# Kernel optimization log

Hardware: AMD Instinct MI355X
Metric: run time of the kernel (lower is better)

## Reference

```python
import jax, jax.numpy as jnp
import numpy as np

B, H, W = 64, 480, 640      # batch, cartesian iris image size
PH, PW = 64, 512            # polar grid
FS, NF = 15, 7              # BSIF filter size / count


def setup_inputs() -> dict:
    key = jax.random.key(0)
    k1, k2, k3, k4, k5, k6 = jax.random.split(key, 6)
    image = jax.random.uniform(k1, (B, 1, H, W), jnp.float32)
    pcx = jax.random.uniform(k2, (B,), jnp.float32, 280.0, 360.0)
    pcy = jax.random.uniform(k3, (B,), jnp.float32, 200.0, 280.0)
    pr = jax.random.uniform(k4, (B,), jnp.float32, 30.0, 60.0)
    ir = jax.random.uniform(k5, (B,), jnp.float32, 90.0, 130.0)
    pupil_xyr = jnp.stack([pcx, pcy, pr], axis=-1)
    iris_xyr = jnp.stack([pcx, pcy, ir], axis=-1)
    filter_mat = jax.random.normal(k6, (FS, FS, NF), jnp.float32)
    return {"image": image, "pupil_xyr": pupil_xyr, "iris_xyr": iris_xyr,
            "filter_mat": filter_mat}


def _bilinear_sample(img, gx, gy):
    """torch.nn.functional.grid_sample, mode=bilinear, align_corners=False,
    padding_mode=zeros. img [B,C,H,W]; gx,gy [B,Hg,Wg] normalized coords."""
    _, _, Hi, Wi = img.shape
    x = ((gx + 1.0) * Wi - 1.0) / 2.0
    y = ((gy + 1.0) * Hi - 1.0) / 2.0
    x0 = jnp.floor(x); y0 = jnp.floor(y)
    wx = x - x0; wy = y - y0

    def gather(ix, iy):
        valid = (ix >= 0) & (ix < Wi) & (iy >= 0) & (iy < Hi)
        ixc = jnp.clip(ix, 0, Wi - 1).astype(jnp.int32)
        iyc = jnp.clip(iy, 0, Hi - 1).astype(jnp.int32)
        v = jax.vmap(lambda im, yy, xx: im[:, yy, xx])(img, iyc, ixc)  # [B,C,Hg,Wg]
        return v * valid[:, None].astype(img.dtype)

    v00 = gather(x0, y0); v01 = gather(x0 + 1, y0)
    v10 = gather(x0, y0 + 1); v11 = gather(x0 + 1, y0 + 1)
    wx = wx[:, None]; wy = wy[:, None]  # [B,1,Hg,Wg]
    return (v00 * (1 - wx) * (1 - wy) + v01 * wx * (1 - wy)
            + v10 * (1 - wx) * wy + v11 * wx * wy)


def _forward(image, pupil_xyr, iris_xyr, filter_mat):
    image_scaled = image * 255.0
    _, _, Hc, Wc = image_scaled.shape

    # --- cartToPol: polar sampling grid from pupil/iris circles ---
    theta = 2.0 * jnp.pi * jnp.arange(1, PW + 1, dtype=jnp.float32) / PW
    cosT, sinT = jnp.cos(theta), jnp.sin(theta)                     # [PW]
    pxc = pupil_xyr[:, 0:1] + pupil_xyr[:, 2:3] * cosT[None]        # [B,PW]
    pyc = pupil_xyr[:, 1:2] + pupil_xyr[:, 2:3] * sinT[None]
    ixc = iris_xyr[:, 0:1] + iris_xyr[:, 2:3] * cosT[None]
    iyc = iris_xyr[:, 1:2] + iris_xyr[:, 2:3] * sinT[None]
    radius = jnp.linspace(0.0, 1.0, PH)[:, None]                    # [PH,1]
    xg = (1 - radius)[None] * pxc[:, None, :] + radius[None] * ixc[:, None, :]  # [B,PH,PW]
    yg = (1 - radius)[None] * pyc[:, None, :] + radius[None] * iyc[:, None, :]
    x = jnp.clip(xg, 0.0, Wc - 1.0)
    y = jnp.clip(yg, 0.0, Hc - 1.0)
    x_norm = x / (Wc - 1) * 2.0 - 1.0
    y_norm = y / (Hc - 1) * 2.0 - 1.0
    # module's custom grid_sample pre-transform (half-pixel re-normalization)
    gx = ((x_norm + 1.0) / 2.0 * Wc - 0.5) / (Wc - 1) * 2.0 - 1.0
    gy = ((y_norm + 1.0) / 2.0 * Hc - 0.5) / (Hc - 1) * 2.0 - 1.0
    image_polar = _bilinear_sample(image_scaled, gx, gy)            # [B,1,PH,PW]

    # --- getCodes: toroidal wrap pad + conv filter bank ---
    r = FS // 2
    img_wrap = jnp.pad(image_polar, ((0, 0), (0, 0), (r, r), (r, r)), mode="wrap")
    # torch: moveaxis(filter[None], 3, 0) -> (NF,1,FS,FS), then flip along dim 0
    weight = jnp.flip(jnp.transpose(filter_mat, (2, 0, 1))[:, None, :, :], axis=0)
    codes = jax.lax.conv_general_dilated(
        img_wrap, weight, window_strides=(1, 1), padding="VALID",
        dimension_numbers=("NCHW", "OIHW", "NCHW"))                 # [B,NF,PH,PW]

    # --- gram matrix ---
    a, b, c, d = codes.shape
    feats = codes.reshape(a * b, c * d)
    gram = (feats @ feats.T) / (a * b * c * d)                      # [a*b, a*b]
    return codes, gram, image_polar


def reference(image, pupil_xyr, iris_xyr, filter_mat):
    return _forward(image, pupil_xyr, iris_xyr, filter_mat)
```

## Files before the change

### kernel.cpp

```cpp
#include <hip/hip_runtime.h>
#include <math.h>

#define BB 64
#define HH 480
#define WW 640
#define PH 64
#define PW 512
#define FS 15
#define NF 7
#define RR 7
#define GD 448
#define KTOT 32768

#define GSPL 16
#define KPB (KTOT / GSPL)
#define GSTK 64
#define GNST (KPB / GSTK)
#define GPLW 72

#define FSPL 32
#define FKPB (KTOT / FSPL)
#define GBK 32
#define GNB (FKPB / GBK)
#define PLW 40

#define CJT 32
#define CSP 52
#define CSPD 26
#define CSROWS 79
#define CSY 46

static constexpr long CODES_N = (long)BB * NF * PH * PW;
static constexpr long GRAM_N  = (long)GD * GD;
static constexpr long POLAR_N = (long)BB * PH * PW;
static constexpr size_t BF_BYTES   = (size_t)GD * KTOT * 2;
static constexpr size_t PART_BYTES = (size_t)GSPL * GRAM_N * 4;

typedef __bf16    bf16x4   __attribute__((ext_vector_type(4)));
typedef __bf16    bf16x8   __attribute__((ext_vector_type(8)));
typedef _Float16  f16x8    __attribute__((ext_vector_type(8)));
typedef float     floatx4  __attribute__((ext_vector_type(4)));
typedef float     floatx16 __attribute__((ext_vector_type(16)));

__constant__ int c_by[28] = {0,0,0,0,0,0,0, 1,1,1,1,1,1, 2,2,2,2,2, 3,3,3,3, 4,4,4, 5,5, 6};
__constant__ int c_bx[28] = {0,1,2,3,4,5,6, 1,2,3,4,5,6, 2,3,4,5,6, 3,4,5,6, 4,5,6, 5,6, 6};

__global__ __launch_bounds__(256) void polar_kernel(
        const float* __restrict__ img,
        const float* __restrict__ pupil,
        const float* __restrict__ iris,
        float* __restrict__ polar) {
    int t = blockIdx.x * 256 + threadIdx.x;
    if (t >= (int)POLAR_N) return;
    int j = t & (PW - 1);
    int i = (t >> 9) & (PH - 1);
    int b = t >> 15;

    float theta = 6.2831855f * (float)(j + 1) / (float)PW;
    float s, c;
    __sincosf(theta, &s, &c);

    float pcx = pupil[b * 3 + 0], pcy = pupil[b * 3 + 1], pr = pupil[b * 3 + 2];
    float icx = iris[b * 3 + 0],  icy = iris[b * 3 + 1],  ir = iris[b * 3 + 2];

    float px = pcx + pr * c;
    float py = pcy + pr * s;
    float ix = icx + ir * c;
    float iy = icy + ir * s;

    float r = (float)i / 63.0f;
    float xg = (1.0f - r) * px + r * ix;
    float yg = (1.0f - r) * py + r * iy;

    float x = fminf(fmaxf(xg, 0.0f), (float)(WW - 1));
    float y = fminf(fmaxf(yg, 0.0f), (float)(HH - 1));

    float xn = x / (float)(WW - 1) * 2.0f - 1.0f;
    float gx = ((xn + 1.0f) / 2.0f * (float)WW - 0.5f) / (float)(WW - 1) * 2.0f - 1.0f;
    float xs = ((gx + 1.0f) * (float)WW - 1.0f) / 2.0f;

    float yn = y / (float)(HH - 1) * 2.0f - 1.0f;
    float gy = ((yn + 1.0f) / 2.0f * (float)HH - 0.5f) / (float)(HH - 1) * 2.0f - 1.0f;
    float ys = ((gy + 1.0f) * (float)HH - 1.0f) / 2.0f;

    float x0f = floorf(xs), y0f = floorf(ys);
    float wx = xs - x0f, wy = ys - y0f;
    int x0 = (int)x0f, y0 = (int)y0f;

    const float* im = img + (size_t)b * (HH * WW);
    float v00 = 0.f, v01 = 0.f, v10 = 0.f, v11 = 0.f;
    bool xv0 = (x0 >= 0) & (x0 < WW);
    bool xv1 = (x0 + 1 >= 0) & (x0 + 1 < WW);
    bool yv0 = (y0 >= 0) & (y0 < HH);
    bool yv1 = (y0 + 1 >= 0) & (y0 + 1 < HH);
    if (xv0 & yv0) v00 = im[(size_t)y0 * WW + x0];
    if (xv1 & yv0) v01 = im[(size_t)y0 * WW + x0 + 1];
    if (xv0 & yv1) v10 = im[(size_t)(y0 + 1) * WW + x0];
    if (xv1 & yv1) v11 = im[(size_t)(y0 + 1) * WW + x0 + 1];

    float val = v00 * (1.0f - wx) * (1.0f - wy) + v01 * wx * (1.0f - wy)
              + v10 * (1.0f - wx) * wy          + v11 * wx * wy;
    polar[t] = val * 255.0f;
}

__global__ __launch_bounds__(256) void conv_mfma_kernel(
        const float* __restrict__ polar,
        const float* __restrict__ fm,
        float* __restrict__ codes,
        __bf16* __restrict__ cbf) {
    __shared__ __align__(16) _Float16 stg[CSROWS * CSP];
    __shared__ __align__(16) float outBuf[NF * 16 * CJT];

    int b  = blockIdx.x >> 4;
    int j0 = (blockIdx.x & 15) * CJT;
    int tid  = threadIdx.x;
    int lane = tid & 63;
    int w    = tid >> 6;

    const float* pb = polar + (size_t)b * (PH * PW);

    for (int e = tid; e < CSROWS * CSY; e += 256) {
        int r = e / CSY;
        int y = e - r * CSY;
        int grow = (r - RR) & (PH - 1);
        int gcol = (j0 - RR + y) & (PW - 1);
        stg[r * CSP + y] = (_Float16)pb[grow * PW + gcol];
    }

    uint4* Wb = (uint4*)outBuf;
    for (int slot = tid; slot < 512; slot += 256) {
        int s  = slot >> 6;
        int l  = slot & 63;
        int du = l >> 5;
        int v0 = ((l >> 4) & 1) * 8;
        int n  = l & 15;
        int jd = (n >= NF) ? 1 : 0;
        int o  = n - NF * jd;
        int u  = 2 * s + du;
        f16x8 vv = {};
        #pragma unroll
        for (int e2 = 0; e2 < 8; ++e2) {
            int v  = v0 + e2;
            int vp = v - jd;
            float wv = 0.0f;
            if (n < 2 * NF && u < FS && vp >= 0 && vp < FS)
                wv = fm[(u * FS + vp) * NF + (NF - 1 - o)];
            vv[e2] = (_Float16)wv;
        }
        Wb[slot] = *(const uint4*)&vv;
    }
    __syncthreads();

    f16x8 Wreg[8];
    #pragma unroll
    for (int s = 0; s < 8; ++s)
        Wreg[s] = *(const f16x8*)&Wb[s * 64 + lane];
    __syncthreads();

    const unsigned int* stg32 = (const unsigned int*)stg;
    int mrow = lane & 15;
    int du   = lane >> 5;
    int v0h  = ((lane >> 4) & 1) * 4;
    int n    = lane & 15;
    int jd   = (n >= NF) ? 1 : 0;
    int o    = n - NF * jd;
    int g4   = lane >> 4;

    for (int it = 0; it < 4; ++it) {
        int i0 = it * 16;
        int rbase = i0 + mrow + du;
        floatx4 acc0 = {}, acc1 = {}, acc2 = {}, acc3 = {};
        #pragma unroll
        for (int s = 0; s < 8; ++s) {
            int dbase = CSPD * (rbase + 2 * s) + 4 * w + v0h;
            uint2 u01 = *(const uint2*)&stg32[dbase + 0];
            uint2 u23 = *(const uint2*)&stg32[dbase + 2];
            uint2 u45 = *(const uint2*)&stg32[dbase + 4];
            uint2 u67 = *(const uint2*)&stg32[dbase + 6];
            unsigned int ud0 = u01.x, ud1 = u01.y, ud2 = u23.x, ud3 = u23.y;
            unsigned int ud4 = u45.x, ud5 = u45.y, ud6 = u67.x, ud7 = u67.y;
            uint4 a0 = make_uint4(ud0, ud1, ud2, ud3);
            uint4 a1 = make_uint4(ud1, ud2, ud3, ud4);
            uint4 a2 = make_uint4(ud2, ud3, ud4, ud5);
            uint4 a3 = make_uint4(ud3, ud4, ud5, ud6);
            (void)ud7;
            acc0 = __builtin_amdgcn_mfma_f32_16x16x32_f16(*(const f16x8*)&a0, Wreg[s], acc0, 0, 0, 0);
            acc1 = __builtin_amdgcn_mfma_f32_16x16x32_f16(*(const f16x8*)&a1, Wreg[s], acc1, 0, 0, 0);
            acc2 = __builtin_amdgcn_mfma_f32_16x16x32_f16(*(const f16x8*)&a2, Wreg[s], acc2, 0, 0, 0);
            acc3 = __builtin_amdgcn_mfma_f32_16x16x32_f16(*(const f16x8*)&a3, Wreg[s], acc3, 0, 0, 0);
        }
        if (n < 2 * NF) {
            #pragma unroll
            for (int r = 0; r < 4; ++r) {
                int orow = (o * 16 + (4 * g4 + r)) * CJT;
                outBuf[orow + 2 * (w * 4 + 0) + jd] = acc0[r];
                outBuf[orow + 2 * (w * 4 + 1) + jd] = acc1[r];
                outBuf[orow + 2 * (w * 4 + 2) + jd] = acc2[r];
                outBuf[orow + 2 * (w * 4 + 3) + jd] = acc3[r];
            }
        }
        __syncthreads();
        for (int g = tid; g < NF * 16 * (CJT / 4); g += 256) {
            int oo  = g >> 7;
            int rem = g & 127;
            int il  = rem >> 3;
            int j4  = rem & 7;
            float4 v = *(const float4*)&outBuf[(oo * 16 + il) * CJT + j4 * 4];
            size_t gbase = (((size_t)b * NF + oo) * PH + i0 + il) * PW + j0 + j4 * 4;
            *(float4*)&codes[gbase] = v;
            if (cbf) {
                bf16x4 bv;
                bv[0] = (__bf16)v.x; bv[1] = (__bf16)v.y;
                bv[2] = (__bf16)v.z; bv[3] = (__bf16)v.w;
                *(bf16x4*)&cbf[gbase] = bv;
            }
        }
        __syncthreads();
    }
}

__global__ __launch_bounds__(256) void gram_bf_kernel(
        const __bf16* __restrict__ feats,
        float* __restrict__ partials) {
    __shared__ __bf16 Ab[2][64][GPLW];
    __shared__ __bf16 Bb[2][64][GPLW];

    int pi = blockIdx.x;
    int by = c_by[pi], bx = c_bx[pi];
    int p0 = by * 64, q0 = bx * 64;
    size_t kbase = (size_t)blockIdx.y * KPB;

    int tid = threadIdx.x;
    int lane = tid & 63;
    int w = tid >> 6;
    int wr = w >> 1, wc = w & 1;

    int srow = tid >> 3;
    int slot = tid & 7;
    const __bf16* apA  = feats + (size_t)(p0 + srow) * KTOT + kbase + slot * 8;
    const __bf16* apA2 = apA + (size_t)32 * KTOT;
    const __bf16* apB  = feats + (size_t)(q0 + srow) * KTOT + kbase + slot * 8;
    const __bf16* apB2 = apB + (size_t)32 * KTOT;

    int arow = 32 * wr + (lane & 31);
    int brow = 32 * wc + (lane & 31);
    int ko = (lane >> 5) * 8;

    floatx16 acc = {};

    bf16x8 ra0 = *(const bf16x8*)(apA);
    bf16x8 ra1 = *(const bf16x8*)(apA2);
    bf16x8 rb0 = *(const bf16x8*)(apB);
    bf16x8 rb1 = *(const bf16x8*)(apB2);
    bf16x8 na0 = *(const bf16x8*)(apA + GSTK);
    bf16x8 na1 = *(const bf16x8*)(apA2 + GSTK);
    bf16x8 nb0 = *(const bf16x8*)(apB + GSTK);
    bf16x8 nb1 = *(const bf16x8*)(apB2 + GSTK);

    for (int s = 0; s < GNST; ++s) {
        int p = s & 1;
        *(bf16x8*)&Ab[p][srow][slot * 8]      = ra0;
        *(bf16x8*)&Ab[p][srow + 32][slot * 8] = ra1;
        *(bf16x8*)&Bb[p][srow][slot * 8]      = rb0;
        *(bf16x8*)&Bb[p][srow + 32][slot * 8] = rb1;
        __syncthreads();
        ra0 = na0; ra1 = na1; rb0 = nb0; rb1 = nb1;
        if (s + 2 < GNST) {
            size_t off = (size_t)(s + 2) * GSTK;
            na0 = *(const bf16x8*)(apA + off);
            na1 = *(const bf16x8*)(apA2 + off);
            nb0 = *(const bf16x8*)(apB + off);
            nb1 = *(const bf16x8*)(apB2 + off);
        }
        #pragma unroll
        for (int st = 0; st < 4; ++st) {
            bf16x8 af = *(const bf16x8*)&Ab[p][arow][st * 16 + ko];
            bf16x8 bg = *(const bf16x8*)&Bb[p][brow][st * 16 + ko];
            acc = __builtin_amdgcn_mfma_f32_32x32x16_bf16(af, bg, acc, 0, 0, 0);
        }
    }

    float* part = partials + (size_t)blockIdx.y * GRAM_N;
    int col = lane & 31;
    #pragma unroll
    for (int r = 0; r < 16; ++r) {
        int row = (r & 3) + 8 * (r >> 2) + 4 * (lane >> 5);
        int p = p0 + 32 * wr + row;
        int q = q0 + 32 * wc + col;
        float v = acc[r];
        part[(size_t)p * GD + q] = v;
        if (bx != by) part[(size_t)q * GD + p] = v;
    }
}

__global__ __launch_bounds__(256) void gram_reduce_kernel(
        const float* __restrict__ partials,
        float* __restrict__ gram) {
    int t = blockIdx.x * 256 + threadIdx.x;
    const float scale = 1.0f / 14680064.0f;
    float4 s = make_float4(0.f, 0.f, 0.f, 0.f);
    #pragma unroll
    for (int sp = 0; sp < GSPL; ++sp) {
        float4 v = *(const float4*)&partials[(size_t)sp * GRAM_N + (size_t)t * 4];
        s.x += v.x; s.y += v.y; s.z += v.z; s.w += v.w;
    }
    s.x *= scale; s.y *= scale; s.z *= scale; s.w *= scale;
    *(float4*)&gram[(size_t)t * 4] = s;
}

__device__ __forceinline__ void split4(float4 v, bf16x4& h, bf16x4& l) {
    float x[4] = {v.x, v.y, v.z, v.w};
    #pragma unroll
    for (int j = 0; j < 4; ++j) {
        __bf16 hh = (__bf16)x[j];
        h[j] = hh;
        l[j] = (__bf16)(x[j] - (float)hh);
    }
}

__global__ __launch_bounds__(256) void gram_hilo_kernel(
        const float* __restrict__ feats,
        float* __restrict__ gram) {
    __shared__ __bf16 Ah[2][64][PLW], Al[2][64][PLW];
    __shared__ __bf16 Bh[2][64][PLW], Bl[2][64][PLW];

    int pi = blockIdx.x;
    int by = c_by[pi], bx = c_bx[pi];
    int p0 = by * 64, q0 = bx * 64;
    int kbase = blockIdx.y * FKPB;

    int tid = threadIdx.x;
    int lane = tid & 63;
    int w = tid >> 6;
    int wr = w >> 1, wc = w & 1;

    int r0 = tid >> 3;
    int slot = tid & 7;
    const float* ap0 = feats + (size_t)(p0 + r0)      * KTOT + kbase + slot * 4;
    const float* ap1 = feats + (size_t)(p0 + r0 + 32) * KTOT + kbase + slot * 4;
    const float* bp0 = feats + (size_t)(q0 + r0)      * KTOT + kbase + slot * 4;
    const float* bp1 = feats + (size_t)(q0 + r0 + 32) * KTOT + kbase + slot * 4;

    int frow = lane & 31;
    int arow = 32 * wr + frow;
    int brow = 32 * wc + frow;
    int kq = (lane >> 5) * 8;

    floatx16 acc = {};

    {
        float4 a0 = *(const float4*)ap0;
        float4 a1 = *(const float4*)ap1;
        float4 b0 = *(const float4*)bp0;
        float4 b1 = *(const float4*)bp1;
        bf16x4 h, l;
        split4(a0, h, l); *(bf16x4*)&Ah[0][r0][slot*4] = h;      *(bf16x4*)&Al[0][r0][slot*4] = l;
        split4(a1, h, l); *(bf16x4*)&Ah[0][r0+32][slot*4] = h;   *(bf16x4*)&Al[0][r0+32][slot*4] = l;
        split4(b0, h, l); *(bf16x4*)&Bh[0][r0][slot*4] = h;      *(bf16x4*)&Bl[0][r0][slot*4] = l;
        split4(b1, h, l); *(bf16x4*)&Bh[0][r0+32][slot*4] = h;   *(bf16x4*)&Bl[0][r0+32][slot*4] = l;
    }
    __syncthreads();

    for (int s = 0; s < GNB; ++s) {
        int buf = s & 1;
        float4 a0, a1, b0, b1;
        if (s + 1 < GNB) {
            int off = (s + 1) * GBK;
            a0 = *(const float4*)(ap0 + off);
            a1 = *(const float4*)(ap1 + off);
            b0 = *(const float4*)(bp0 + off);
            b1 = *(const float4*)(bp1 + off);
        }
        #pragma unroll
        for (int kk = 0; kk < 2; ++kk) {
            int ko = kq + kk * 16;
            bf16x8 ah = *(const bf16x8*)&Ah[buf][arow][ko];
            bf16x8 al = *(const bf16x8*)&Al[buf][arow][ko];
            bf16x8 bh = *(const bf16x8*)&Bh[buf][brow][ko];
            bf16x8 bl = *(const bf16x8*)&Bl[buf][brow][ko];
            acc = __builtin_amdgcn_mfma_f32_32x32x16_bf16(ah, bh, acc, 0, 0, 0);
            acc = __builtin_amdgcn_mfma_f32_32x32x16_bf16(ah, bl, acc, 0, 0, 0);
            acc = __builtin_amdgcn_mfma_f32_32x32x16_bf16(al, bh, acc, 0, 0, 0);
        }
        if (s + 1 < GNB) {
            int nb = (s + 1) & 1;
            bf16x4 h, l;
            split4(a0, h, l); *(bf16x4*)&Ah[nb][r0][slot*4] = h;      *(bf16x4*)&Al[nb][r0][slot*4] = l;
            split4(a1, h, l); *(bf16x4*)&Ah[nb][r0+32][slot*4] = h;   *(bf16x4*)&Al[nb][r0+32][slot*4] = l;
            split4(b0, h, l); *(bf16x4*)&Bh[nb][r0][slot*4] = h;      *(bf16x4*)&Bl[nb][r0][slot*4] = l;
            split4(b1, h, l); *(bf16x4*)&Bh[nb][r0+32][slot*4] = h;   *(bf16x4*)&Bl[nb][r0+32][slot*4] = l;
        }
        __syncthreads();
    }

    const float scale = 1.0f / 14680064.0f;
    int col = lane & 31;
    #pragma unroll
    for (int r = 0; r < 16; ++r) {
        int row = (r & 3) + 8 * (r >> 2) + 4 * (lane >> 5);
        int p = p0 + 32 * wr + row;
        int q = q0 + 32 * wc + col;
        float v = acc[r] * scale;
        atomicAdd(&gram[(size_t)p * GD + q], v);
        if (bx != by) atomicAdd(&gram[(size_t)q * GD + p], v);
    }
}

extern "C" void kernel_launch(void* const* d_in, const int* in_sizes, int n_in,
                              void* d_out, int out_size, void* d_ws, size_t ws_size,
                              hipStream_t stream) {
    const float* img   = (const float*)d_in[0];
    const float* pupil = (const float*)d_in[1];
    const float* iris  = (const float*)d_in[2];
    const float* fm    = (const float*)d_in[3];

    float* codes = (float*)d_out;
    float* gram  = codes + CODES_N;
    float* polar = gram + GRAM_N;

    bool use_bf = (ws_size >= BF_BYTES + PART_BYTES);
    __bf16* cbf = use_bf ? (__bf16*)d_ws : nullptr;
    float* partials = (float*)((char*)d_ws + BF_BYTES);

    polar_kernel<<<(int)(POLAR_N / 256), 256, 0, stream>>>(img, pupil, iris, polar);

    conv_mfma_kernel<<<BB * (PW / CJT), 256, 0, stream>>>(polar, fm, codes, cbf);

    if (use_bf) {
        dim3 ggrid(28, GSPL);
        gram_bf_kernel<<<ggrid, 256, 0, stream>>>((const __bf16*)d_ws, partials);
        gram_reduce_kernel<<<(int)(GRAM_N / 4 / 256), 256, 0, stream>>>(partials, gram);
    } else {
        hipMemsetAsync(gram, 0, GRAM_N * sizeof(float), stream);
        dim3 ggrid(28, FSPL);
        gram_hilo_kernel<<<ggrid, 28 * FSPL == 0 ? 256 : 256, 0, stream>>>(codes, gram);
    }
}
```

Before: 203.7 us.

## Split conv blocks over row tiles, precompute weight fragments, double gram K-split

The conv kernel now launches one block per (batch, column tile, 16-row tile) rather than looping over four row tiles, so the staging buffer shrinks to 31 rows and the grid grows fourfold. The MFMA weight fragments are built once by block 0 of the polar kernel into a workspace table, so conv blocks no longer recompute them from the filter matrix. The gram K-split is doubled to 32 and the LDS row padding is changed. The finer conv split re-stages overlapping halo rows (31 rows per 16 output rows), and the doubled gram split makes the partials buffer and its reduction larger.

```diff
diff --git a/kernel.cpp b/kernel.cpp
--- a/kernel.cpp
+++ b/kernel.cpp
@@ -12,11 +12,11 @@
 #define GD 448
 #define KTOT 32768
 
-#define GSPL 16
+#define GSPL 32
 #define KPB (KTOT / GSPL)
 #define GSTK 64
 #define GNST (KPB / GSTK)
-#define GPLW 72
+#define GPLW 66
 
 #define FSPL 32
 #define FKPB (KTOT / FSPL)
@@ -27,7 +27,7 @@
 #define CJT 32
 #define CSP 52
 #define CSPD 26
-#define CSROWS 79
+#define CSROWS 31
 #define CSY 46
 
 static constexpr long CODES_N = (long)BB * NF * PH * PW;
@@ -35,6 +35,7 @@
 static constexpr long POLAR_N = (long)BB * PH * PW;
 static constexpr size_t BF_BYTES   = (size_t)GD * KTOT * 2;
 static constexpr size_t PART_BYTES = (size_t)GSPL * GRAM_N * 4;
+static constexpr size_t WTAB_BYTES = 512 * 16;
 
 typedef __bf16    bf16x4   __attribute__((ext_vector_type(4)));
 typedef __bf16    bf16x8   __attribute__((ext_vector_type(8)));
@@ -45,11 +46,40 @@
 __constant__ int c_by[28] = {0,0,0,0,0,0,0, 1,1,1,1,1,1, 2,2,2,2,2, 3,3,3,3, 4,4,4, 5,5, 6};
 __constant__ int c_bx[28] = {0,1,2,3,4,5,6, 1,2,3,4,5,6, 2,3,4,5,6, 3,4,5,6, 4,5,6, 5,6, 6};
 
+__device__ __forceinline__ float wfrag_val(const float* fm, int s, int l, int e) {
+    int du = l >> 5;
+    int v0 = ((l >> 4) & 1) * 8;
+    int n  = l & 15;
+    int jd = (n >= NF) ? 1 : 0;
+    int o  = n - NF * jd;
+    int u  = 2 * s + du;
+    int v  = v0 + e;
+    int vp = v - jd;
+    float wv = 0.0f;
+    if (n < 2 * NF && u < FS && vp >= 0 && vp < FS)
+        wv = fm[(u * FS + vp) * NF + (NF - 1 - o)];
+    return wv;
+}
+
 __global__ __launch_bounds__(256) void polar_kernel(
         const float* __restrict__ img,
         const float* __restrict__ pupil,
         const float* __restrict__ iris,
-        float* __restrict__ polar) {
+        const float* __restrict__ fm,
+        float* __restrict__ polar,
+        _Float16* __restrict__ wtab) {
+    if (wtab && blockIdx.x == 0) {
+        #pragma unroll
+        for (int ss = 0; ss < 2; ++ss) {
+            int slot = threadIdx.x + ss * 256;
+            int s = slot >> 6, l = slot & 63;
+            f16x8 vv;
+            #pragma unroll
+            for (int e = 0; e < 8; ++e) vv[e] = (_Float16)wfrag_val(fm, s, l, e);
+            *(f16x8*)&wtab[slot * 8] = vv;
+        }
+    }
+
     int t = blockIdx.x * 256 + threadIdx.x;
     if (t >= (int)POLAR_N) return;
     int j = t & (PW - 1);
@@ -106,13 +136,18 @@
 __global__ __launch_bounds__(256) void conv_mfma_kernel(
         const float* __restrict__ polar,
         const float* __restrict__ fm,
+        const _Float16* __restrict__ wtab,
         float* __restrict__ codes,
         __bf16* __restrict__ cbf) {
     __shared__ __align__(16) _Float16 stg[CSROWS * CSP];
     __shared__ __align__(16) float outBuf[NF * 16 * CJT];
 
-    int b  = blockIdx.x >> 4;
-    int j0 = (blockIdx.x & 15) * CJT;
+    int bid = blockIdx.x;
+    int b   = bid >> 6;
+    int jt  = (bid >> 2) & 15;
+    int it  = bid & 3;
+    int j0  = jt * CJT;
+    int i0  = it * 16;
     int tid  = threadIdx.x;
     int lane = tid & 63;
     int w    = tid >> 6;
@@ -122,40 +157,32 @@
     for (int e = tid; e < CSROWS * CSY; e += 256) {
         int r = e / CSY;
         int y = e - r * CSY;
-        int grow = (r - RR) & (PH - 1);
+        int grow = (i0 + r - RR) & (PH - 1);
         int gcol = (j0 - RR + y) & (PW - 1);
         stg[r * CSP + y] = (_Float16)pb[grow * PW + gcol];
     }
 
-    uint4* Wb = (uint4*)outBuf;
-    for (int slot = tid; slot < 512; slot += 256) {
-        int s  = slot >> 6;
-        int l  = slot & 63;
-        int du = l >> 5;
-        int v0 = ((l >> 4) & 1) * 8;
-        int n  = l & 15;
-        int jd = (n >= NF) ? 1 : 0;
-        int o  = n - NF * jd;
-        int u  = 2 * s + du;
-        f16x8 vv = {};
-        #pragma unroll
-        for (int e2 = 0; e2 < 8; ++e2) {
-            int v  = v0 + e2;
-            int vp = v - jd;
-            float wv = 0.0f;
-            if (n < 2 * NF && u < FS && vp >= 0 && vp < FS)
-                wv = fm[(u * FS + vp) * NF + (NF - 1 - o)];
-            vv[e2] = (_Float16)wv;
-        }
-        Wb[slot] = *(const uint4*)&vv;
-    }
-    __syncthreads();
-
     f16x8 Wreg[8];
-    #pragma unroll
-    for (int s = 0; s < 8; ++s)
-        Wreg[s] = *(const f16x8*)&Wb[s * 64 + lane];
-    __syncthreads();
+    if (wtab) {
+        #pragma unroll
+        for (int s = 0; s < 8; ++s)
+            Wreg[s] = *(const f16x8*)&wtab[(s * 64 + lane) * 8];
+        __syncthreads();
+    } else {
+        uint4* Wb = (uint4*)outBuf;
+        for (int slot = tid; slot < 512; slot += 256) {
+            int s = slot >> 6, l = slot & 63;
+            f16x8 vv;
+            #pragma unroll
+            for (int e2 = 0; e2 < 8; ++e2) vv[e2] = (_Float16)wfrag_val(fm, s, l, e2);
+            Wb[slot] = *(const uint4*)&vv;
+        }
+        __syncthreads();
+        #pragma unroll
+        for (int s = 0; s < 8; ++s)
+            Wreg[s] = *(const f16x8*)&Wb[s * 64 + lane];
+        __syncthreads();
+    }
 
     const unsigned int* stg32 = (const unsigned int*)stg;
     int mrow = lane & 15;
@@ -166,56 +193,51 @@
     int o    = n - NF * jd;
     int g4   = lane >> 4;
 
-    for (int it = 0; it < 4; ++it) {
-        int i0 = it * 16;
-        int rbase = i0 + mrow + du;
-        floatx4 acc0 = {}, acc1 = {}, acc2 = {}, acc3 = {};
-        #pragma unroll
-        for (int s = 0; s < 8; ++s) {
-            int dbase = CSPD * (rbase + 2 * s) + 4 * w + v0h;
-            uint2 u01 = *(const uint2*)&stg32[dbase + 0];
-            uint2 u23 = *(const uint2*)&stg32[dbase + 2];
-            uint2 u45 = *(const uint2*)&stg32[dbase + 4];
-            uint2 u67 = *(const uint2*)&stg32[dbase + 6];
-            unsigned int ud0 = u01.x, ud1 = u01.y, ud2 = u23.x, ud3 = u23.y;
-            unsigned int ud4 = u45.x, ud5 = u45.y, ud6 = u67.x, ud7 = u67.y;
-            uint4 a0 = make_uint4(ud0, ud1, ud2, ud3);
-            uint4 a1 = make_uint4(ud1, ud2, ud3, ud4);
-            uint4 a2 = make_uint4(ud2, ud3, ud4, ud5);
-            uint4 a3 = make_uint4(ud3, ud4, ud5, ud6);
-            (void)ud7;
-            acc0 = __builtin_amdgcn_mfma_f32_16x16x32_f16(*(const f16x8*)&a0, Wreg[s], acc0, 0, 0, 0);
-            acc1 = __builtin_amdgcn_mfma_f32_16x16x32_f16(*(const f16x8*)&a1, Wreg[s], acc1, 0, 0, 0);
-            acc2 = __builtin_amdgcn_mfma_f32_16x16x32_f16(*(const f16x8*)&a2, Wreg[s], acc2, 0, 0, 0);
-            acc3 = __builtin_amdgcn_mfma_f32_16x16x32_f16(*(const f16x8*)&a3, Wreg[s], acc3, 0, 0, 0);
-        }
-        if (n < 2 * NF) {
-            #pragma unroll
-            for (int r = 0; r < 4; ++r) {
-                int orow = (o * 16 + (4 * g4 + r)) * CJT;
-                outBuf[orow + 2 * (w * 4 + 0) + jd] = acc0[r];
-                outBuf[orow + 2 * (w * 4 + 1) + jd] = acc1[r];
-                outBuf[orow + 2 * (w * 4 + 2) + jd] = acc2[r];
-                outBuf[orow + 2 * (w * 4 + 3) + jd] = acc3[r];
-            }
-        }
-        __syncthreads();
-        for (int g = tid; g < NF * 16 * (CJT / 4); g += 256) {
-            int oo  = g >> 7;
-            int rem = g & 127;
-            int il  = rem >> 3;
-            int j4  = rem & 7;
-            float4 v = *(const float4*)&outBuf[(oo * 16 + il) * CJT + j4 * 4];
-            size_t gbase = (((size_t)b * NF + oo) * PH + i0 + il) * PW + j0 + j4 * 4;
-            *(float4*)&codes[gbase] = v;
-            if (cbf) {
-                bf16x4 bv;
-                bv[0] = (__bf16)v.x; bv[1] = (__bf16)v.y;
-                bv[2] = (__bf16)v.z; bv[3] = (__bf16)v.w;
-                *(bf16x4*)&cbf[gbase] = bv;
-            }
-        }
-        __syncthreads();
+    floatx4 acc0 = {}, acc1 = {}, acc2 = {}, acc3 = {};
+    #pragma unroll
+    for (int s = 0; s < 8; ++s) {
+        int dbase = CSPD * (mrow + du + 2 * s) + 4 * w + v0h;
+        uint2 u01 = *(const uint2*)&stg32[dbase + 0];
+        uint2 u23 = *(const uint2*)&stg32[dbase + 2];
+        uint2 u45 = *(const uint2*)&stg32[dbase + 4];
+        uint2 u67 = *(const uint2*)&stg32[dbase + 6];
+        unsigned int ud0 = u01.x, ud1 = u01.y, ud2 = u23.x, ud3 = u23.y;
+        unsigned int ud4 = u45.x, ud5 = u45.y, ud6 = u67.x, ud7 = u67.y;
+        uint4 a0 = make_uint4(ud0, ud1, ud2, ud3);
+        uint4 a1 = make_uint4(ud1, ud2, ud3, ud4);
+        uint4 a2 = make_uint4(ud2, ud3, ud4, ud5);
+        uint4 a3 = make_uint4(ud3, ud4, ud5, ud6);
+        (void)ud7;
+        acc0 = __builtin_amdgcn_mfma_f32_16x16x32_f16(*(const f16x8*)&a0, Wreg[s], acc0, 0, 0, 0);
+        acc1 = __builtin_amdgcn_mfma_f32_16x16x32_f16(*(const f16x8*)&a1, Wreg[s], acc1, 0, 0, 0);
+        acc2 = __builtin_amdgcn_mfma_f32_16x16x32_f16(*(const f16x8*)&a2, Wreg[s], acc2, 0, 0, 0);
+        acc3 = __builtin_amdgcn_mfma_f32_16x16x32_f16(*(const f16x8*)&a3, Wreg[s], acc3, 0, 0, 0);
+    }
+    if (n < 2 * NF) {
+        #pragma unroll
+        for (int r = 0; r < 4; ++r) {
+            int orow = (o * 16 + (4 * g4 + r)) * CJT;
+            outBuf[orow + 2 * (w * 4 + 0) + jd] = acc0[r];
+            outBuf[orow + 2 * (w * 4 + 1) + jd] = acc1[r];
+            outBuf[orow + 2 * (w * 4 + 2) + jd] = acc2[r];
+            outBuf[orow + 2 * (w * 4 + 3) + jd] = acc3[r];
+        }
+    }
+    __syncthreads();
+    for (int g = tid; g < NF * 16 * (CJT / 4); g += 256) {
+        int oo  = g >> 7;
+        int rem = g & 127;
+        int il  = rem >> 3;
+        int j4  = rem & 7;
+        float4 v = *(const float4*)&outBuf[(oo * 16 + il) * CJT + j4 * 4];
+        size_t gbase = (((size_t)b * NF + oo) * PH + i0 + il) * PW + j0 + j4 * 4;
+        *(float4*)&codes[gbase] = v;
+        if (cbf) {
+            bf16x4 bv;
+            bv[0] = (__bf16)v.x; bv[1] = (__bf16)v.y;
+            bv[2] = (__bf16)v.z; bv[3] = (__bf16)v.w;
+            *(bf16x4*)&cbf[gbase] = bv;
+        }
     }
 }
 
@@ -418,13 +440,14 @@
     float* gram  = codes + CODES_N;
     float* polar = gram + GRAM_N;
 
-    bool use_bf = (ws_size >= BF_BYTES + PART_BYTES);
+    bool use_bf = (ws_size >= BF_BYTES + PART_BYTES + WTAB_BYTES);
     __bf16* cbf = use_bf ? (__bf16*)d_ws : nullptr;
     float* partials = (float*)((char*)d_ws + BF_BYTES);
-
-    polar_kernel<<<(int)(POLAR_N / 256), 256, 0, stream>>>(img, pupil, iris, polar);
-
-    conv_mfma_kernel<<<BB * (PW / CJT), 256, 0, stream>>>(polar, fm, codes, cbf);
+    _Float16* wtab = use_bf ? (_Float16*)((char*)d_ws + BF_BYTES + PART_BYTES) : nullptr;
+
+    polar_kernel<<<(int)(POLAR_N / 256), 256, 0, stream>>>(img, pupil, iris, fm, polar, wtab);
+
+    conv_mfma_kernel<<<BB * 16 * 4, 256, 0, stream>>>(polar, fm, wtab, codes, cbf);
 
     if (use_bf) {
         dim3 ggrid(28, GSPL);
@@ -433,6 +456,6 @@
     } else {
         hipMemsetAsync(gram, 0, GRAM_N * sizeof(float), stream);
         dim3 ggrid(28, FSPL);
-        gram_hilo_kernel<<<ggrid, 28 * FSPL == 0 ? 256 : 256, 0, stream>>>(codes, gram);
-    }
-}
+        gram_hilo_kernel<<<ggrid, 256, 0, stream>>>(codes, gram);
+    }
+}
```

Measured after the change: 206.7 us. About the same (+1.5%).
